# Kernel tuning notes

Hardware: AMD Instinct MI355X
Metric: run time of the kernel (lower is better)

## Reference

```python
import jax, jax.numpy as jnp
import numpy as np

E, D, H, K, N = 8, 512, 2048, 2, 1024  # experts, d_model, d_hidden, top_k, tokens
EPS = 1e-5


def _moe_linear(x, idx, W, b):
    # x: (M, in); idx: (M,) expert id per row; W: (E, out, in); b: (E, out)
    # Brute-force: compute per-expert dense GEMMs, select via one-hot (matches
    # BruteForceMoELinear math: y[i] = x[i] @ W[idx[i]].T + b[idx[i]]).
    m = jax.nn.one_hot(idx, W.shape[0], dtype=x.dtype)  # (M, E)
    y = jnp.einsum('me,eoi,mi->mo', m, W, x)
    return y + jnp.take(b, idx, axis=0)


def _forward(inp, gate_w, gate_b, w1, b1, w2, b2, ln_w, ln_b):
    # NaiveGate: linear -> top_k -> softmax over top-k logits
    logits = inp @ gate_w.T + gate_b              # (N, E)
    top_val, top_idx = jax.lax.top_k(logits, K)   # (N, K)
    score = jax.nn.softmax(top_val, axis=-1)      # (N, K)
    # repeat_interleave tokens, dispatch to experts
    x = jnp.repeat(inp, K, axis=0)                # (N*K, D)
    idx = top_idx.reshape(-1)                     # (N*K,)
    x = _moe_linear(x, idx, w1, b1)               # (N*K, H)
    x = jax.nn.gelu(x, approximate=False)         # torch F.gelu default = erf
    x = _moe_linear(x, idx, w2, b2)               # (N*K, D)
    x = x.reshape(N, K, D)
    x = jnp.einsum('nk,nkd->nd', score, x)        # bmm((N,1,K),(N,K,D)) combine
    # post layer norm (pre_lnorm=False)
    mu = jnp.mean(x, axis=-1, keepdims=True)
    var = jnp.var(x, axis=-1, keepdims=True)
    return (x - mu) * jax.lax.rsqrt(var + EPS) * ln_w + ln_b


def setup_inputs() -> dict:
    key = jax.random.key(0)
    ks = jax.random.split(key, 8)
    s = 0.02
    return {
        'inp': jax.random.normal(ks[0], (N, D), dtype=jnp.float32),
        'gate_w': s * jax.random.normal(ks[1], (E, D), dtype=jnp.float32),
        'gate_b': jnp.zeros((E,), dtype=jnp.float32),
        'w1': s * jax.random.normal(ks[2], (E, H, D), dtype=jnp.float32),
        'b1': jnp.zeros((E, H), dtype=jnp.float32),
        'w2': s * jax.random.normal(ks[3], (E, D, H), dtype=jnp.float32),
        'b2': jnp.zeros((E, D), dtype=jnp.float32),
        'ln_w': jnp.ones((D,), dtype=jnp.float32),
        'ln_b': jnp.zeros((D,), dtype=jnp.float32),
    }


def reference(inp, gate_w, gate_b, w1, b1, w2, b2, ln_w, ln_b):
    return _forward(inp, gate_w, gate_b, w1, b1, w2, b2, ln_w, ln_b)
```

## Files before the change

kernel.cpp:

```cpp
#include <hip/hip_runtime.h>
#include <cstdint>
#include <cstddef>

typedef _Float16 half_t;
typedef _Float16 half8 __attribute__((ext_vector_type(8)));
typedef float floatx4 __attribute__((ext_vector_type(4)));

#define E_ 8
#define D_ 512
#define H_ 2048
#define NTOK 1024
#define NP 2048
#define CAP 1024
#define TM 128

__device__ __forceinline__ float gelu_f(float x) {
    return 0.5f * x * (1.0f + erff(x * 0.7071067811865476f));
}

__device__ __forceinline__ void gload_lds16(const half_t* g, half_t* l) {
    __builtin_amdgcn_global_load_lds(
        (__attribute__((address_space(1))) void*)(g),
        (__attribute__((address_space(3))) void*)(l),
        16, 0, 0);
}

__global__ __launch_bounds__(256) void cvt_kernel(
        const float* __restrict__ w1, const float* __restrict__ w2,
        half_t* __restrict__ W1h, half_t* __restrict__ W2h,
        int* __restrict__ cnt_g) {
    if (blockIdx.x == 0 && threadIdx.x < E_) cnt_g[threadIdx.x] = 0;
    const int NG = E_ * H_ * D_ / 8;
    int i = blockIdx.x * 256 + threadIdx.x;
    const float* src; half_t* dst; int j;
    if (i < NG) { src = w1; dst = W1h; j = i; }
    else        { src = w2; dst = W2h; j = i - NG; }
    const floatx4* s = (const floatx4*)src + (size_t)j * 2;
    floatx4 f0 = s[0], f1 = s[1];
    half8 h = { (half_t)f0[0], (half_t)f0[1], (half_t)f0[2], (half_t)f0[3],
                (half_t)f1[0], (half_t)f1[1], (half_t)f1[2], (half_t)f1[3] };
    *(half8*)(dst + (size_t)j * 8) = h;
}

__global__ __launch_bounds__(256) void gate_scatter_kernel(
        const float* __restrict__ inp, const float* __restrict__ gate_w,
        const float* __restrict__ gate_b,
        float* __restrict__ score, int* __restrict__ idx,
        int* __restrict__ pos_of_pair, int* __restrict__ cnt_g,
        half_t* __restrict__ Xg) {
    int n = blockIdx.x * 4 + (threadIdx.x >> 6);
    int lane = threadIdx.x & 63;
    const floatx4* xr = (const floatx4*)(inp + (size_t)n * D_);
    floatx4 x0 = xr[lane * 2], x1 = xr[lane * 2 + 1];
    float l[E_];
    #pragma unroll
    for (int e = 0; e < E_; e++) {
        const floatx4* gr = (const floatx4*)(gate_w + (size_t)e * D_);
        floatx4 g0 = gr[lane * 2], g1 = gr[lane * 2 + 1];
        float p = x0[0]*g0[0] + x0[1]*g0[1] + x0[2]*g0[2] + x0[3]*g0[3]
                + x1[0]*g1[0] + x1[1]*g1[1] + x1[2]*g1[2] + x1[3]*g1[3];
        #pragma unroll
        for (int m = 1; m < 64; m <<= 1) p += __shfl_xor(p, m);
        l[e] = p + gate_b[e];
    }
    int e0 = 0; float v0 = l[0];
    #pragma unroll
    for (int e = 1; e < E_; e++) if (l[e] > v0) { v0 = l[e]; e0 = e; }
    int e1 = -1; float v1 = -3.4e38f;
    #pragma unroll
    for (int e = 0; e < E_; e++) if (e != e0 && l[e] > v1) { v1 = l[e]; e1 = e; }
    int p0 = 0, p1 = 0;
    if (lane == 0) {
        float s1 = expf(v1 - v0);
        float den = 1.0f + s1;
        score[2 * n]     = 1.0f / den;
        score[2 * n + 1] = s1 / den;
        idx[2 * n]     = e0;
        idx[2 * n + 1] = e1;
        p0 = e0 * CAP + atomicAdd(&cnt_g[e0], 1);
        p1 = e1 * CAP + atomicAdd(&cnt_g[e1], 1);
        pos_of_pair[2 * n]     = p0;
        pos_of_pair[2 * n + 1] = p1;
    }
    p0 = __shfl(p0, 0);
    p1 = __shfl(p1, 0);
    half8 h = { (half_t)x0[0], (half_t)x0[1], (half_t)x0[2], (half_t)x0[3],
                (half_t)x1[0], (half_t)x1[1], (half_t)x1[2], (half_t)x1[3] };
    *(half8*)(Xg + (size_t)p0 * D_ + lane * 8) = h;
    *(half8*)(Xg + (size_t)p1 * D_ + lane * 8) = h;
}

__global__ __launch_bounds__(256, 2) void gemm1_kernel(
        const half_t* __restrict__ Xg, const half_t* __restrict__ W1h,
        const float* __restrict__ b1, const int* __restrict__ cnt_g,
        half_t* __restrict__ Y1) {
    __shared__ half_t As[2 * 128 * 32];
    __shared__ half_t Bs[2 * 128 * 32];
    int slot = blockIdx.x;
    int e = slot >> 3, ti = slot & 7;
    int valid = cnt_g[e] - ti * TM;
    if (valid <= 0) return;
    int cnt = valid < TM ? valid : TM;
    int row0 = e * CAP + ti * TM;
    int colbase = blockIdx.y * 128;
    int tid = threadIdx.x;
    int wave = tid >> 6, lane = tid & 63, quad = lane >> 4, l16 = lane & 15;
    int wm = (wave & 1) * 64, wn = (wave >> 1) * 64;
    const half_t* Abase = Xg + (size_t)row0 * D_;
    const half_t* Bbase = W1h + ((size_t)e * H_ + colbase) * D_;
    int srow = tid >> 2, scol = (tid & 3) * 8;
    floatx4 acc[4][4] = {};
    for (int k0 = 0; k0 < D_; k0 += 64) {
        __syncthreads();
        #pragma unroll
        for (int j = 0; j < 2; j++) {
            #pragma unroll
            for (int s = 0; s < 2; s++) {
                int q = tid + s * 256;
                int row = srow + s * 64;
                gload_lds16(Abase + (size_t)row * D_ + k0 + j * 32 + scol,
                            As + j * 4096 + q * 8);
                gload_lds16(Bbase + (size_t)row * D_ + k0 + j * 32 + scol,
                            Bs + j * 4096 + q * 8);
            }
        }
        __syncthreads();
        #pragma unroll
        for (int j = 0; j < 2; j++) {
            half8 a[4], b[4];
            #pragma unroll
            for (int mi = 0; mi < 4; mi++)
                a[mi] = *(const half8*)(As + j * 4096 + (wm + mi * 16 + l16) * 32 + quad * 8);
            #pragma unroll
            for (int ni = 0; ni < 4; ni++)
                b[ni] = *(const half8*)(Bs + j * 4096 + (wn + ni * 16 + l16) * 32 + quad * 8);
            #pragma unroll
            for (int mi = 0; mi < 4; mi++)
                #pragma unroll
                for (int ni = 0; ni < 4; ni++)
                    acc[mi][ni] = __builtin_amdgcn_mfma_f32_16x16x32_f16(a[mi], b[ni], acc[mi][ni], 0, 0, 0);
        }
    }
    float bias[4];
    #pragma unroll
    for (int ni = 0; ni < 4; ni++)
        bias[ni] = b1[(size_t)e * H_ + colbase + wn + ni * 16 + l16];
    #pragma unroll
    for (int mi = 0; mi < 4; mi++) {
        #pragma unroll
        for (int r = 0; r < 4; r++) {
            int rr = wm + mi * 16 + quad * 4 + r;
            if (rr >= cnt) continue;
            size_t rowoff = (size_t)(row0 + rr) * H_;
            #pragma unroll
            for (int ni = 0; ni < 4; ni++) {
                float v = acc[mi][ni][r] + bias[ni];
                Y1[rowoff + colbase + wn + ni * 16 + l16] = (half_t)gelu_f(v);
            }
        }
    }
}

__global__ __launch_bounds__(256, 2) void gemm2_kernel(
        const half_t* __restrict__ Y1, const half_t* __restrict__ W2h,
        const int* __restrict__ cnt_g, float* __restrict__ Y2p) {
    __shared__ half_t As[2 * 128 * 32];
    __shared__ half_t Bs[2 * 128 * 32];
    int slot = blockIdx.x;
    int e = slot >> 3, ti = slot & 7;
    int valid = cnt_g[e] - ti * TM;
    if (valid <= 0) return;
    int cnt = valid < TM ? valid : TM;
    int row0 = e * CAP + ti * TM;
    int colbase = blockIdx.y * 128;
    int kz = blockIdx.z;
    int kzb = kz * 512;
    int tid = threadIdx.x;
    int wave = tid >> 6, lane = tid & 63, quad = lane >> 4, l16 = lane & 15;
    int wm = (wave & 1) * 64, wn = (wave >> 1) * 64;
    const half_t* Abase = Y1 + (size_t)row0 * H_ + kzb;
    const half_t* Bbase = W2h + ((size_t)e * D_ + colbase) * H_ + kzb;
    int srow = tid >> 2, scol = (tid & 3) * 8;
    floatx4 acc[4][4] = {};
    for (int k0 = 0; k0 < 512; k0 += 64) {
        __syncthreads();
        #pragma unroll
        for (int j = 0; j < 2; j++) {
            #pragma unroll
            for (int s = 0; s < 2; s++) {
                int q = tid + s * 256;
                int row = srow + s * 64;
                gload_lds16(Abase + (size_t)row * H_ + k0 + j * 32 + scol,
                            As + j * 4096 + q * 8);
                gload_lds16(Bbase + (size_t)row * H_ + k0 + j * 32 + scol,
                            Bs + j * 4096 + q * 8);
            }
        }
        __syncthreads();
        #pragma unroll
        for (int j = 0; j < 2; j++) {
            half8 a[4], b[4];
            #pragma unroll
            for (int mi = 0; mi < 4; mi++)
                a[mi] = *(const half8*)(As + j * 4096 + (wm + mi * 16 + l16) * 32 + quad * 8);
            #pragma unroll
            for (int ni = 0; ni < 4; ni++)
                b[ni] = *(const half8*)(Bs + j * 4096 + (wn + ni * 16 + l16) * 32 + quad * 8);
            #pragma unroll
            for (int mi = 0; mi < 4; mi++)
                #pragma unroll
                for (int ni = 0; ni < 4; ni++)
                    acc[mi][ni] = __builtin_amdgcn_mfma_f32_16x16x32_f16(a[mi], b[ni], acc[mi][ni], 0, 0, 0);
        }
    }
    #pragma unroll
    for (int mi = 0; mi < 4; mi++) {
        #pragma unroll
        for (int r = 0; r < 4; r++) {
            int rr = wm + mi * 16 + quad * 4 + r;
            if (rr >= cnt) continue;
            size_t rowoff = ((size_t)kz * (E_ * CAP) + row0 + rr) * D_;
            #pragma unroll
            for (int ni = 0; ni < 4; ni++)
                Y2p[rowoff + colbase + wn + ni * 16 + l16] = acc[mi][ni][r];
        }
    }
}

__global__ __launch_bounds__(256) void final_kernel(
        const float* __restrict__ Y2p, const float* __restrict__ b2,
        const int* __restrict__ idx, const float* __restrict__ score,
        const int* __restrict__ pos_of_pair,
        const float* __restrict__ ln_w, const float* __restrict__ ln_b,
        float* __restrict__ out) {
    int n = blockIdx.x * 4 + (threadIdx.x >> 6);
    int lane = threadIdx.x & 63;
    int p0 = pos_of_pair[2 * n], p1 = pos_of_pair[2 * n + 1];
    int e0 = idx[2 * n], e1 = idx[2 * n + 1];
    float s0 = score[2 * n], s1 = score[2 * n + 1];

    const floatx4* b2r0 = (const floatx4*)(b2 + (size_t)e0 * D_);
    const floatx4* b2r1 = (const floatx4*)(b2 + (size_t)e1 * D_);
    floatx4 a_lo = b2r0[lane * 2], a_hi = b2r0[lane * 2 + 1];
    floatx4 c_lo = b2r1[lane * 2], c_hi = b2r1[lane * 2 + 1];
    #pragma unroll
    for (int kz = 0; kz < 4; kz++) {
        const floatx4* r0 = (const floatx4*)(Y2p + ((size_t)kz * (E_ * CAP) + p0) * D_);
        const floatx4* r1 = (const floatx4*)(Y2p + ((size_t)kz * (E_ * CAP) + p1) * D_);
        a_lo += r0[lane * 2]; a_hi += r0[lane * 2 + 1];
        c_lo += r1[lane * 2]; c_hi += r1[lane * 2 + 1];
    }
    floatx4 y_lo = s0 * a_lo + s1 * c_lo;
    floatx4 y_hi = s0 * a_hi + s1 * c_hi;

    float s = 0.0f, q = 0.0f;
    #pragma unroll
    for (int j = 0; j < 4; j++) {
        s += y_lo[j] + y_hi[j];
        q += y_lo[j] * y_lo[j] + y_hi[j] * y_hi[j];
    }
    #pragma unroll
    for (int m = 1; m < 64; m <<= 1) {
        s += __shfl_xor(s, m);
        q += __shfl_xor(q, m);
    }
    float mean = s * (1.0f / 512.0f);
    float var = q * (1.0f / 512.0f) - mean * mean;
    float inv = 1.0f / sqrtf(var + 1e-5f);

    const floatx4* wv = (const floatx4*)ln_w;
    const floatx4* bv = (const floatx4*)ln_b;
    floatx4 o_lo = (y_lo - mean) * inv * wv[lane * 2]     + bv[lane * 2];
    floatx4 o_hi = (y_hi - mean) * inv * wv[lane * 2 + 1] + bv[lane * 2 + 1];
    floatx4* op = (floatx4*)(out + (size_t)n * D_);
    op[lane * 2] = o_lo;
    op[lane * 2 + 1] = o_hi;
}

extern "C" void kernel_launch(void* const* d_in, const int* in_sizes, int n_in,
                              void* d_out, int out_size, void* d_ws, size_t ws_size,
                              hipStream_t stream) {
    const float* inp    = (const float*)d_in[0];
    const float* gate_w = (const float*)d_in[1];
    const float* gate_b = (const float*)d_in[2];
    const float* w1     = (const float*)d_in[3];
    const float* b1     = (const float*)d_in[4];
    const float* w2     = (const float*)d_in[5];
    const float* b2     = (const float*)d_in[6];
    const float* ln_w   = (const float*)d_in[7];
    const float* ln_b   = (const float*)d_in[8];
    float* out = (float*)d_out;

    char* ws = (char*)d_ws;
    size_t o = 0;
    auto carve = [&](size_t bytes) -> char* {
        char* p = ws + o;
        o += (bytes + 255) & ~(size_t)255;
        return p;
    };
    half_t* W1h = (half_t*)carve(sizeof(half_t) * (size_t)E_ * H_ * D_);
    half_t* W2h = (half_t*)carve(sizeof(half_t) * (size_t)E_ * D_ * H_);
    half_t* Xg  = (half_t*)carve(sizeof(half_t) * (size_t)E_ * CAP * D_);
    half_t* Y1  = (half_t*)carve(sizeof(half_t) * (size_t)E_ * CAP * H_);
    float*  Y2p = (float*)carve(sizeof(float) * 4 * (size_t)E_ * CAP * D_);
    float*  score = (float*)carve(sizeof(float) * NP);
    int* idx         = (int*)carve(sizeof(int) * NP);
    int* pos_of_pair = (int*)carve(sizeof(int) * NP);
    int* cnt_g       = (int*)carve(sizeof(int) * E_);

    cvt_kernel<<<2 * E_ * H_ * D_ / 8 / 256, 256, 0, stream>>>(w1, w2, W1h, W2h, cnt_g);
    gate_scatter_kernel<<<NTOK / 4, 256, 0, stream>>>(inp, gate_w, gate_b,
                                                      score, idx, pos_of_pair, cnt_g, Xg);
    gemm1_kernel<<<dim3(E_ * (CAP / TM), H_ / 128), 256, 0, stream>>>(
        Xg, W1h, b1, cnt_g, Y1);
    gemm2_kernel<<<dim3(E_ * (CAP / TM), D_ / 128, 4), 256, 0, stream>>>(
        Y1, W2h, cnt_g, Y2p);
    final_kernel<<<NTOK / 4, 256, 0, stream>>>(Y2p, b2, idx, score, pos_of_pair, ln_w, ln_b, out);
}
```

Measured before the change: 206.6 us.

## Fuse weight conversion with gating, double-buffer GEMM tiles, shrink M tile

Merges the fp32→fp16 weight conversion and the gate/scatter step into one grid-stride kernel, and moves the expert-counter reset to a memset. Both expert GEMMs now double-buffer their LDS tiles, loading the next K slice while computing the current one, which removes one barrier per iteration. The M tile shrinks from 128 to 64 rows so more blocks run and less work is wasted on partly filled expert tiles, with occupancy raised to 3 blocks per CU. The smaller tile lowers reuse of the B operand per block, and the fused kernel serialises the gate work inside the conversion blocks.

```diff
diff --git a/kernel.cpp b/kernel.cpp
--- a/kernel.cpp
+++ b/kernel.cpp
@@ -12,7 +12,8 @@
 #define NTOK 1024
 #define NP 2048
 #define CAP 1024
-#define TM 128
+#define TM1 64
+#define TN1 128
 
 __device__ __forceinline__ float gelu_f(float x) {
     return 0.5f * x * (1.0f + erff(x * 0.7071067811865476f));
@@ -25,128 +26,137 @@
         16, 0, 0);
 }
 
-__global__ __launch_bounds__(256) void cvt_kernel(
+__global__ __launch_bounds__(256) void cvt_gate_kernel(
         const float* __restrict__ w1, const float* __restrict__ w2,
         half_t* __restrict__ W1h, half_t* __restrict__ W2h,
-        int* __restrict__ cnt_g) {
-    if (blockIdx.x == 0 && threadIdx.x < E_) cnt_g[threadIdx.x] = 0;
-    const int NG = E_ * H_ * D_ / 8;
-    int i = blockIdx.x * 256 + threadIdx.x;
-    const float* src; half_t* dst; int j;
-    if (i < NG) { src = w1; dst = W1h; j = i; }
-    else        { src = w2; dst = W2h; j = i - NG; }
-    const floatx4* s = (const floatx4*)src + (size_t)j * 2;
-    floatx4 f0 = s[0], f1 = s[1];
-    half8 h = { (half_t)f0[0], (half_t)f0[1], (half_t)f0[2], (half_t)f0[3],
-                (half_t)f1[0], (half_t)f1[1], (half_t)f1[2], (half_t)f1[3] };
-    *(half8*)(dst + (size_t)j * 8) = h;
-}
-
-__global__ __launch_bounds__(256) void gate_scatter_kernel(
         const float* __restrict__ inp, const float* __restrict__ gate_w,
         const float* __restrict__ gate_b,
         float* __restrict__ score, int* __restrict__ idx,
         int* __restrict__ pos_of_pair, int* __restrict__ cnt_g,
         half_t* __restrict__ Xg) {
-    int n = blockIdx.x * 4 + (threadIdx.x >> 6);
-    int lane = threadIdx.x & 63;
-    const floatx4* xr = (const floatx4*)(inp + (size_t)n * D_);
-    floatx4 x0 = xr[lane * 2], x1 = xr[lane * 2 + 1];
-    float l[E_];
-    #pragma unroll
-    for (int e = 0; e < E_; e++) {
-        const floatx4* gr = (const floatx4*)(gate_w + (size_t)e * D_);
-        floatx4 g0 = gr[lane * 2], g1 = gr[lane * 2 + 1];
-        float p = x0[0]*g0[0] + x0[1]*g0[1] + x0[2]*g0[2] + x0[3]*g0[3]
-                + x1[0]*g1[0] + x1[1]*g1[1] + x1[2]*g1[2] + x1[3]*g1[3];
-        #pragma unroll
-        for (int m = 1; m < 64; m <<= 1) p += __shfl_xor(p, m);
-        l[e] = p + gate_b[e];
-    }
-    int e0 = 0; float v0 = l[0];
-    #pragma unroll
-    for (int e = 1; e < E_; e++) if (l[e] > v0) { v0 = l[e]; e0 = e; }
-    int e1 = -1; float v1 = -3.4e38f;
-    #pragma unroll
-    for (int e = 0; e < E_; e++) if (e != e0 && l[e] > v1) { v1 = l[e]; e1 = e; }
-    int p0 = 0, p1 = 0;
-    if (lane == 0) {
-        float s1 = expf(v1 - v0);
-        float den = 1.0f + s1;
-        score[2 * n]     = 1.0f / den;
-        score[2 * n + 1] = s1 / den;
-        idx[2 * n]     = e0;
-        idx[2 * n + 1] = e1;
-        p0 = e0 * CAP + atomicAdd(&cnt_g[e0], 1);
-        p1 = e1 * CAP + atomicAdd(&cnt_g[e1], 1);
-        pos_of_pair[2 * n]     = p0;
-        pos_of_pair[2 * n + 1] = p1;
-    }
-    p0 = __shfl(p0, 0);
-    p1 = __shfl(p1, 0);
-    half8 h = { (half_t)x0[0], (half_t)x0[1], (half_t)x0[2], (half_t)x0[3],
-                (half_t)x1[0], (half_t)x1[1], (half_t)x1[2], (half_t)x1[3] };
-    *(half8*)(Xg + (size_t)p0 * D_ + lane * 8) = h;
-    *(half8*)(Xg + (size_t)p1 * D_ + lane * 8) = h;
-}
-
-__global__ __launch_bounds__(256, 2) void gemm1_kernel(
+    const int blk = blockIdx.x, tid = threadIdx.x;
+    if (blk < NTOK / 4) {
+        int n = blk * 4 + (tid >> 6);
+        int lane = tid & 63;
+        const floatx4* xr = (const floatx4*)(inp + (size_t)n * D_);
+        floatx4 x0 = xr[lane * 2], x1 = xr[lane * 2 + 1];
+        float l[E_];
+        #pragma unroll
+        for (int e = 0; e < E_; e++) {
+            const floatx4* gr = (const floatx4*)(gate_w + (size_t)e * D_);
+            floatx4 g0 = gr[lane * 2], g1 = gr[lane * 2 + 1];
+            float p = x0[0]*g0[0] + x0[1]*g0[1] + x0[2]*g0[2] + x0[3]*g0[3]
+                    + x1[0]*g1[0] + x1[1]*g1[1] + x1[2]*g1[2] + x1[3]*g1[3];
+            #pragma unroll
+            for (int m = 1; m < 64; m <<= 1) p += __shfl_xor(p, m);
+            l[e] = p + gate_b[e];
+        }
+        int e0 = 0; float v0 = l[0];
+        #pragma unroll
+        for (int e = 1; e < E_; e++) if (l[e] > v0) { v0 = l[e]; e0 = e; }
+        int e1 = -1; float v1 = -3.4e38f;
+        #pragma unroll
+        for (int e = 0; e < E_; e++) if (e != e0 && l[e] > v1) { v1 = l[e]; e1 = e; }
+        int p0 = 0, p1 = 0;
+        if (lane == 0) {
+            float s1 = expf(v1 - v0);
+            float den = 1.0f + s1;
+            score[2 * n]     = 1.0f / den;
+            score[2 * n + 1] = s1 / den;
+            idx[2 * n]     = e0;
+            idx[2 * n + 1] = e1;
+            p0 = e0 * CAP + atomicAdd(&cnt_g[e0], 1);
+            p1 = e1 * CAP + atomicAdd(&cnt_g[e1], 1);
+            pos_of_pair[2 * n]     = p0;
+            pos_of_pair[2 * n + 1] = p1;
+        }
+        p0 = __shfl(p0, 0);
+        p1 = __shfl(p1, 0);
+        half8 h = { (half_t)x0[0], (half_t)x0[1], (half_t)x0[2], (half_t)x0[3],
+                    (half_t)x1[0], (half_t)x1[1], (half_t)x1[2], (half_t)x1[3] };
+        *(half8*)(Xg + (size_t)p0 * D_ + lane * 8) = h;
+        *(half8*)(Xg + (size_t)p1 * D_ + lane * 8) = h;
+    }
+    const int NG = E_ * H_ * D_ / 8;
+    for (int i = blk * 256 + tid; i < 2 * NG; i += gridDim.x * 256) {
+        const float* src; half_t* dst; int j;
+        if (i < NG) { src = w1; dst = W1h; j = i; }
+        else        { src = w2; dst = W2h; j = i - NG; }
+        const floatx4* s = (const floatx4*)src + (size_t)j * 2;
+        floatx4 f0 = s[0], f1 = s[1];
+        half8 h = { (half_t)f0[0], (half_t)f0[1], (half_t)f0[2], (half_t)f0[3],
+                    (half_t)f1[0], (half_t)f1[1], (half_t)f1[2], (half_t)f1[3] };
+        *(half8*)(dst + (size_t)j * 8) = h;
+    }
+}
+
+__device__ __forceinline__ void stage_tile(const half_t* Abase, const half_t* Bbase,
+                                           half_t* As, half_t* Bs,
+                                           int k0, int buf, int tid,
+                                           int strideA, int strideB) {
+    int row = tid >> 2, col8 = (tid & 3) * 8;
+    #pragma unroll
+    for (int j = 0; j < 2; j++) {
+        gload_lds16(Abase + (size_t)row * strideA + k0 + j * 32 + col8,
+                    As + buf * 4096 + j * 2048 + tid * 8);
+        #pragma unroll
+        for (int s = 0; s < 2; s++) {
+            int q = tid + s * 256;
+            gload_lds16(Bbase + (size_t)(row + s * 64) * strideB + k0 + j * 32 + col8,
+                        Bs + buf * 8192 + j * 4096 + q * 8);
+        }
+    }
+}
+
+__global__ __launch_bounds__(256, 3) void gemm1_kernel(
         const half_t* __restrict__ Xg, const half_t* __restrict__ W1h,
         const float* __restrict__ b1, const int* __restrict__ cnt_g,
         half_t* __restrict__ Y1) {
-    __shared__ half_t As[2 * 128 * 32];
-    __shared__ half_t Bs[2 * 128 * 32];
+    __shared__ half_t As[2 * 2 * 64 * 32];
+    __shared__ half_t Bs[2 * 2 * 128 * 32];
     int slot = blockIdx.x;
-    int e = slot >> 3, ti = slot & 7;
-    int valid = cnt_g[e] - ti * TM;
+    int e = slot >> 4, ti = slot & 15;
+    int valid = cnt_g[e] - ti * TM1;
     if (valid <= 0) return;
-    int cnt = valid < TM ? valid : TM;
-    int row0 = e * CAP + ti * TM;
-    int colbase = blockIdx.y * 128;
+    int cnt = valid < TM1 ? valid : TM1;
+    int row0 = e * CAP + ti * TM1;
+    int colbase = blockIdx.y * TN1;
     int tid = threadIdx.x;
     int wave = tid >> 6, lane = tid & 63, quad = lane >> 4, l16 = lane & 15;
-    int wm = (wave & 1) * 64, wn = (wave >> 1) * 64;
+    int wm = (wave & 1) * 32, wn = (wave >> 1) * 64;
     const half_t* Abase = Xg + (size_t)row0 * D_;
     const half_t* Bbase = W1h + ((size_t)e * H_ + colbase) * D_;
-    int srow = tid >> 2, scol = (tid & 3) * 8;
-    floatx4 acc[4][4] = {};
-    for (int k0 = 0; k0 < D_; k0 += 64) {
+
+    floatx4 acc[2][4] = {};
+    int buf = 0;
+    stage_tile(Abase, Bbase, As, Bs, 0, 0, tid, D_, D_);
+    for (int it = 0; it < 8; it++) {
         __syncthreads();
+        if (it < 7)
+            stage_tile(Abase, Bbase, As, Bs, (it + 1) * 64, buf ^ 1, tid, D_, D_);
         #pragma unroll
         for (int j = 0; j < 2; j++) {
-            #pragma unroll
-            for (int s = 0; s < 2; s++) {
-                int q = tid + s * 256;
-                int row = srow + s * 64;
-                gload_lds16(Abase + (size_t)row * D_ + k0 + j * 32 + scol,
-                            As + j * 4096 + q * 8);
-                gload_lds16(Bbase + (size_t)row * D_ + k0 + j * 32 + scol,
-                            Bs + j * 4096 + q * 8);
-            }
-        }
-        __syncthreads();
-        #pragma unroll
-        for (int j = 0; j < 2; j++) {
-            half8 a[4], b[4];
-            #pragma unroll
-            for (int mi = 0; mi < 4; mi++)
-                a[mi] = *(const half8*)(As + j * 4096 + (wm + mi * 16 + l16) * 32 + quad * 8);
+            half8 a[2], b[4];
+            #pragma unroll
+            for (int mi = 0; mi < 2; mi++)
+                a[mi] = *(const half8*)(As + buf * 4096 + j * 2048 + (wm + mi * 16 + l16) * 32 + quad * 8);
             #pragma unroll
             for (int ni = 0; ni < 4; ni++)
-                b[ni] = *(const half8*)(Bs + j * 4096 + (wn + ni * 16 + l16) * 32 + quad * 8);
-            #pragma unroll
-            for (int mi = 0; mi < 4; mi++)
+                b[ni] = *(const half8*)(Bs + buf * 8192 + j * 4096 + (wn + ni * 16 + l16) * 32 + quad * 8);
+            #pragma unroll
+            for (int mi = 0; mi < 2; mi++)
                 #pragma unroll
                 for (int ni = 0; ni < 4; ni++)
                     acc[mi][ni] = __builtin_amdgcn_mfma_f32_16x16x32_f16(a[mi], b[ni], acc[mi][ni], 0, 0, 0);
         }
+        buf ^= 1;
     }
     float bias[4];
     #pragma unroll
     for (int ni = 0; ni < 4; ni++)
         bias[ni] = b1[(size_t)e * H_ + colbase + wn + ni * 16 + l16];
     #pragma unroll
-    for (int mi = 0; mi < 4; mi++) {
+    for (int mi = 0; mi < 2; mi++) {
         #pragma unroll
         for (int r = 0; r < 4; r++) {
             int rr = wm + mi * 16 + quad * 4 + r;
@@ -161,60 +171,51 @@
     }
 }
 
-__global__ __launch_bounds__(256, 2) void gemm2_kernel(
+__global__ __launch_bounds__(256, 3) void gemm2_kernel(
         const half_t* __restrict__ Y1, const half_t* __restrict__ W2h,
         const int* __restrict__ cnt_g, float* __restrict__ Y2p) {
-    __shared__ half_t As[2 * 128 * 32];
-    __shared__ half_t Bs[2 * 128 * 32];
+    __shared__ half_t As[2 * 2 * 64 * 32];
+    __shared__ half_t Bs[2 * 2 * 128 * 32];
     int slot = blockIdx.x;
-    int e = slot >> 3, ti = slot & 7;
-    int valid = cnt_g[e] - ti * TM;
+    int e = slot >> 4, ti = slot & 15;
+    int valid = cnt_g[e] - ti * TM1;
     if (valid <= 0) return;
-    int cnt = valid < TM ? valid : TM;
-    int row0 = e * CAP + ti * TM;
-    int colbase = blockIdx.y * 128;
-    int kz = blockIdx.z;
-    int kzb = kz * 512;
+    int cnt = valid < TM1 ? valid : TM1;
+    int row0 = e * CAP + ti * TM1;
+    int colbase = blockIdx.y * TN1;
+    int kz = blockIdx.z, kzb = kz * 512;
     int tid = threadIdx.x;
     int wave = tid >> 6, lane = tid & 63, quad = lane >> 4, l16 = lane & 15;
-    int wm = (wave & 1) * 64, wn = (wave >> 1) * 64;
+    int wm = (wave & 1) * 32, wn = (wave >> 1) * 64;
     const half_t* Abase = Y1 + (size_t)row0 * H_ + kzb;
     const half_t* Bbase = W2h + ((size_t)e * D_ + colbase) * H_ + kzb;
-    int srow = tid >> 2, scol = (tid & 3) * 8;
-    floatx4 acc[4][4] = {};
-    for (int k0 = 0; k0 < 512; k0 += 64) {
+
+    floatx4 acc[2][4] = {};
+    int buf = 0;
+    stage_tile(Abase, Bbase, As, Bs, 0, 0, tid, H_, H_);
+    for (int it = 0; it < 8; it++) {
         __syncthreads();
+        if (it < 7)
+            stage_tile(Abase, Bbase, As, Bs, (it + 1) * 64, buf ^ 1, tid, H_, H_);
         #pragma unroll
         for (int j = 0; j < 2; j++) {
-            #pragma unroll
-            for (int s = 0; s < 2; s++) {
-                int q = tid + s * 256;
-                int row = srow + s * 64;
-                gload_lds16(Abase + (size_t)row * H_ + k0 + j * 32 + scol,
-                            As + j * 4096 + q * 8);
-                gload_lds16(Bbase + (size_t)row * H_ + k0 + j * 32 + scol,
-                            Bs + j * 4096 + q * 8);
-            }
-        }
-        __syncthreads();
-        #pragma unroll
-        for (int j = 0; j < 2; j++) {
-            half8 a[4], b[4];
-            #pragma unroll
-            for (int mi = 0; mi < 4; mi++)
-                a[mi] = *(const half8*)(As + j * 4096 + (wm + mi * 16 + l16) * 32 + quad * 8);
+            half8 a[2], b[4];
+            #pragma unroll
+            for (int mi = 0; mi < 2; mi++)
+                a[mi] = *(const half8*)(As + buf * 4096 + j * 2048 + (wm + mi * 16 + l16) * 32 + quad * 8);
             #pragma unroll
             for (int ni = 0; ni < 4; ni++)
-                b[ni] = *(const half8*)(Bs + j * 4096 + (wn + ni * 16 + l16) * 32 + quad * 8);
-            #pragma unroll
-            for (int mi = 0; mi < 4; mi++)
+                b[ni] = *(const half8*)(Bs + buf * 8192 + j * 4096 + (wn + ni * 16 + l16) * 32 + quad * 8);
+            #pragma unroll
+            for (int mi = 0; mi < 2; mi++)
                 #pragma unroll
                 for (int ni = 0; ni < 4; ni++)
                     acc[mi][ni] = __builtin_amdgcn_mfma_f32_16x16x32_f16(a[mi], b[ni], acc[mi][ni], 0, 0, 0);
         }
-    }
-    #pragma unroll
-    for (int mi = 0; mi < 4; mi++) {
+        buf ^= 1;
+    }
+    #pragma unroll
+    for (int mi = 0; mi < 2; mi++) {
         #pragma unroll
         for (int r = 0; r < 4; r++) {
             int rr = wm + mi * 16 + quad * 4 + r;
@@ -308,12 +309,13 @@
     int* pos_of_pair = (int*)carve(sizeof(int) * NP);
     int* cnt_g       = (int*)carve(sizeof(int) * E_);
 
-    cvt_kernel<<<2 * E_ * H_ * D_ / 8 / 256, 256, 0, stream>>>(w1, w2, W1h, W2h, cnt_g);
-    gate_scatter_kernel<<<NTOK / 4, 256, 0, stream>>>(inp, gate_w, gate_b,
-                                                      score, idx, pos_of_pair, cnt_g, Xg);
-    gemm1_kernel<<<dim3(E_ * (CAP / TM), H_ / 128), 256, 0, stream>>>(
+    hipMemsetAsync(cnt_g, 0, sizeof(int) * E_, stream);
+    cvt_gate_kernel<<<1024, 256, 0, stream>>>(w1, w2, W1h, W2h,
+                                              inp, gate_w, gate_b,
+                                              score, idx, pos_of_pair, cnt_g, Xg);
+    gemm1_kernel<<<dim3(E_ * (CAP / TM1), H_ / TN1), 256, 0, stream>>>(
         Xg, W1h, b1, cnt_g, Y1);
-    gemm2_kernel<<<dim3(E_ * (CAP / TM), D_ / 128, 4), 256, 0, stream>>>(
+    gemm2_kernel<<<dim3(E_ * (CAP / TM1), D_ / TN1, 4), 256, 0, stream>>>(
         Y1, W2h, cnt_g, Y2p);
     final_kernel<<<NTOK / 4, 256, 0, stream>>>(Y2p, b2, idx, score, pos_of_pair, ln_w, ln_b, out);
 }
```

New measurement: 223.3 us. +8.1%, slower.
